# Kernel optimization log

Measured on AMD Instinct MI355X. Metric: run time of the kernel, lower is better.

The kernel has to match this reference:

```python
import jax, jax.numpy as jnp
import numpy as np

D = 4096  # input_size
H = 4096  # hidden_size


def setup_inputs() -> dict:
    key = jax.random.key(0)
    ks = jax.random.split(key, 18)
    inp = {
        "x": jax.random.normal(ks[0], (D,), jnp.float32),
        "h_prev": jax.random.normal(ks[1], (H,), jnp.float32),
        "c_prev": jax.random.normal(ks[2], (H, H), jnp.float32),
        "n_prev": jax.random.normal(ks[3], (H,), jnp.float32),
        "m_prev": jax.random.normal(ks[4], (H,), jnp.float32),
    }
    names = ["q", "k", "v", "i", "f", "o"]
    for idx, nm in enumerate(names):
        inp[f"W{nm}"] = jax.random.normal(ks[5 + 2 * idx], (H, D), jnp.float32) * 0.02
        inp[f"b{nm}"] = jax.random.normal(ks[6 + 2 * idx], (H,), jnp.float32) * 0.02
    return inp


def reference(x, h_prev, c_prev, n_prev, m_prev,
              Wq, bq, Wk, bk, Wv, bv, Wi, bi, Wf, bf, Wo, bo):
    # Six linear projections (nn.Linear: W @ x + b for 1-D x)
    q = Wq @ x + bq
    k = (Wk @ x + bk) / jnp.sqrt(jnp.float32(H))
    v = Wv @ x + bv
    o = jax.nn.sigmoid(Wo @ x + bo)
    i_tilde = Wi @ x + bi
    f_tilde = Wf @ x + bf

    # Stabilizer state and exp gates
    m_t = jnp.maximum(f_tilde + m_prev, i_tilde)          # [H]
    i_g = jnp.exp(i_tilde - m_t)                          # [H]
    f_g = jnp.exp(f_tilde + m_prev - m_t)                 # [H]

    # Rank-1 outer-product state update; gates broadcast over last axis (as in torch)
    c_t = f_g * c_prev + i_g * jnp.outer(v, k)            # [H, H]
    n_t = f_g * n_prev + i_g * k                          # [H]

    # Normalized matvec output
    denom = jnp.maximum(jnp.abs(jnp.dot(n_t, q)), jnp.float32(1.0))
    h_t = o * (c_t @ q) / denom                           # [H]
    return (h_t, c_t, n_t, m_t)
```

## Files before the change

### kernel.cpp

```cpp
#include <hip/hip_runtime.h>
#include <math.h>

#define HD 4096

__global__ __launch_bounds__(256, 6) void k_gemv(
    const float* __restrict__ x,
    const float* __restrict__ Wq, const float* __restrict__ Wk,
    const float* __restrict__ Wv, const float* __restrict__ Wi,
    const float* __restrict__ Wf, const float* __restrict__ Wo,
    float* __restrict__ ws_dots)
{
    __shared__ float xs[HD];
    const int tid = threadIdx.x;
    {
        const float4* x4  = (const float4*)x;
        float4*       sx4 = (float4*)xs;
#pragma unroll
        for (int i = 0; i < 4; ++i) sx4[i * 256 + tid] = x4[i * 256 + tid];
    }
    __syncthreads();

    const int wave = tid >> 6;
    const int lane = tid & 63;
    const int mat  = blockIdx.x >> 10;
    const int row  = ((blockIdx.x & 1023) << 2) | wave;

    const float* W = Wq;
    if      (mat == 1) W = Wk;
    else if (mat == 2) W = Wv;
    else if (mat == 3) W = Wi;
    else if (mat == 4) W = Wf;
    else if (mat == 5) W = Wo;

    const float4* Wrow = (const float4*)(W + (size_t)row * HD) + lane;
    const float4* sx4  = (const float4*)xs + lane;

    float a0 = 0.f, a1 = 0.f;
#pragma unroll
    for (int t = 0; t < 16; t += 2) {
        float4 w0 = Wrow[t * 64];
        float4 x0 = sx4[t * 64];
        float4 w1 = Wrow[(t + 1) * 64];
        float4 x1 = sx4[(t + 1) * 64];
        a0 += w0.x * x0.x + w0.y * x0.y + w0.z * x0.z + w0.w * x0.w;
        a1 += w1.x * x1.x + w1.y * x1.y + w1.z * x1.z + w1.w * x1.w;
    }
    float acc = a0 + a1;
#pragma unroll
    for (int off = 32; off > 0; off >>= 1)
        acc += __shfl_xor(acc, off, 64);

    if (lane == 0) ws_dots[(mat << 12) | row] = acc;
}

__global__ __launch_bounds__(256) void k_gates(
    const float* __restrict__ ws_dots,
    const float* __restrict__ bq, const float* __restrict__ bk,
    const float* __restrict__ bv, const float* __restrict__ bi,
    const float* __restrict__ bf, const float* __restrict__ bo,
    const float* __restrict__ n_prev, const float* __restrict__ m_prev,
    float* __restrict__ ws_q, float* __restrict__ ws_v,
    float* __restrict__ ws_o, float* __restrict__ ws_fg,
    float* __restrict__ ws_ik,
    float* __restrict__ out_n, float* __restrict__ out_m,
    float* __restrict__ ws_nq)
{
    const int tid = threadIdx.x;
    const int row = blockIdx.x * 256 + tid;

    float dq  = ws_dots[0 * HD + row];
    float dk  = ws_dots[1 * HD + row];
    float dv  = ws_dots[2 * HD + row];
    float di  = ws_dots[3 * HD + row];
    float df  = ws_dots[4 * HD + row];
    float d_o = ws_dots[5 * HD + row];

    float q  = dq + bq[row];
    float k  = (dk + bk[row]) * (1.0f / 64.0f);
    float v  = dv + bv[row];
    float o  = 1.0f / (1.0f + expf(-(d_o + bo[row])));
    float it = di + bi[row];
    float ft = df + bf[row];
    float mp = m_prev[row];
    float mt = fmaxf(ft + mp, it);
    float ig = expf(it - mt);
    float fg = expf(ft + mp - mt);
    float nt = fg * n_prev[row] + ig * k;

    ws_q[row]  = q;
    ws_v[row]  = v;
    ws_o[row]  = o;
    ws_fg[row] = fg;
    ws_ik[row] = ig * k;
    out_n[row] = nt;
    out_m[row] = mt;

    float acc = nt * q;
#pragma unroll
    for (int off = 32; off > 0; off >>= 1)
        acc += __shfl_xor(acc, off, 64);
    __shared__ float red[4];
    if ((tid & 63) == 0) red[tid >> 6] = acc;
    __syncthreads();
    if (tid == 0) ws_nq[blockIdx.x] = red[0] + red[1] + red[2] + red[3];
}

__global__ __launch_bounds__(256) void k_ct(
    const float* __restrict__ c_prev,
    const float* __restrict__ ws_q, const float* __restrict__ ws_v,
    const float* __restrict__ ws_o, const float* __restrict__ ws_fg,
    const float* __restrict__ ws_ik, const float* __restrict__ ws_nq,
    float* __restrict__ out_h, float* __restrict__ out_c)
{
    const int row = blockIdx.x;
    const int tid = threadIdx.x;
    const float vr = ws_v[row];

    const float4* cp4 = (const float4*)(c_prev + (size_t)row * HD);
    float4*       ct4 = (float4*)(out_c + (size_t)row * HD);
    const float4* fg4 = (const float4*)ws_fg;
    const float4* ik4 = (const float4*)ws_ik;
    const float4* q4  = (const float4*)ws_q;

    float4 c[4], f[4], k[4], qv[4];
#pragma unroll
    for (int t = 0; t < 4; ++t) {
        const int idx = t * 256 + tid;
        c[t]  = cp4[idx];
        f[t]  = fg4[idx];
        k[t]  = ik4[idx];
        qv[t] = q4[idx];
    }

    float acc = 0.f;
#pragma unroll
    for (int t = 0; t < 4; ++t) {
        const int idx = t * 256 + tid;
        float4 ct;
        ct.x = f[t].x * c[t].x + k[t].x * vr;
        ct.y = f[t].y * c[t].y + k[t].y * vr;
        ct.z = f[t].z * c[t].z + k[t].z * vr;
        ct.w = f[t].w * c[t].w + k[t].w * vr;
        ct4[idx] = ct;
        acc += ct.x * qv[t].x + ct.y * qv[t].y + ct.z * qv[t].z + ct.w * qv[t].w;
    }
#pragma unroll
    for (int off = 32; off > 0; off >>= 1)
        acc += __shfl_xor(acc, off, 64);
    __shared__ float red[4];
    if ((tid & 63) == 0) red[tid >> 6] = acc;
    __syncthreads();
    if (tid == 0) {
        float s = red[0] + red[1] + red[2] + red[3];
        float d = 0.f;
#pragma unroll
        for (int i = 0; i < 16; ++i) d += ws_nq[i];
        float den = fmaxf(fabsf(d), 1.0f);
        out_h[row] = ws_o[row] * s / den;
    }
}

extern "C" void kernel_launch(void* const* d_in, const int* in_sizes, int n_in,
                              void* d_out, int out_size, void* d_ws, size_t ws_size,
                              hipStream_t stream) {
    const float* x      = (const float*)d_in[0];
    const float* c_prev = (const float*)d_in[2];
    const float* n_prev = (const float*)d_in[3];
    const float* m_prev = (const float*)d_in[4];
    const float* Wq = (const float*)d_in[5];  const float* bq = (const float*)d_in[6];
    const float* Wk = (const float*)d_in[7];  const float* bk = (const float*)d_in[8];
    const float* Wv = (const float*)d_in[9];  const float* bv = (const float*)d_in[10];
    const float* Wi = (const float*)d_in[11]; const float* bi = (const float*)d_in[12];
    const float* Wf = (const float*)d_in[13]; const float* bf = (const float*)d_in[14];
    const float* Wo = (const float*)d_in[15]; const float* bo = (const float*)d_in[16];

    float* out   = (float*)d_out;
    float* out_h = out;
    float* out_c = out + HD;
    float* out_n = out + HD + (size_t)HD * HD;
    float* out_m = out_n + HD;

    float* ws      = (float*)d_ws;
    float* ws_dots = ws;
    float* ws_q    = ws + 6 * HD;
    float* ws_v    = ws + 7 * HD;
    float* ws_o    = ws + 8 * HD;
    float* ws_fg   = ws + 9 * HD;
    float* ws_ik   = ws + 10 * HD;
    float* ws_nq   = ws + 11 * HD;

    k_gemv<<<6 * 1024, 256, 0, stream>>>(x, Wq, Wk, Wv, Wi, Wf, Wo, ws_dots);
    k_gates<<<16, 256, 0, stream>>>(ws_dots, bq, bk, bv, bi, bf, bo,
                                    n_prev, m_prev,
                                    ws_q, ws_v, ws_o, ws_fg, ws_ik,
                                    out_n, out_m, ws_nq);
    k_ct<<<HD, 256, 0, stream>>>(c_prev, ws_q, ws_v, ws_o, ws_fg, ws_ik,
                                 ws_nq, out_h, out_c);
}
```

Before: 437.1 us.

## Stream GEMV weights through double-buffered LDS via direct global-to-LDS loads

The projection GEMV now gives each wave four rows and keeps x in registers instead of shared memory. Weight chunks are streamed into per-wave double-buffered LDS with global_load_lds, using explicit waitcnt so the next chunk loads while the current one is reduced. The grid shrinks from 6144 to 1536 blocks and the launch-bounds occupancy hint drops from 6 to 4. This raises register use (16 float4 of x per thread) and relies on hand-written waitcnt ordering, which is fragile.

```diff
diff --git a/kernel.cpp b/kernel.cpp
--- a/kernel.cpp
+++ b/kernel.cpp
@@ -3,27 +3,27 @@
 
 #define HD 4096
 
-__global__ __launch_bounds__(256, 6) void k_gemv(
+__device__ __forceinline__ void gload16(const float* g, float* l) {
+    __builtin_amdgcn_global_load_lds(
+        (const __attribute__((address_space(1))) void*)g,
+        (__attribute__((address_space(3))) void*)l,
+        16, 0, 0);
+}
+
+__global__ __launch_bounds__(256, 4) void k_gemv(
     const float* __restrict__ x,
     const float* __restrict__ Wq, const float* __restrict__ Wk,
     const float* __restrict__ Wv, const float* __restrict__ Wi,
     const float* __restrict__ Wf, const float* __restrict__ Wo,
     float* __restrict__ ws_dots)
 {
-    __shared__ float xs[HD];
-    const int tid = threadIdx.x;
-    {
-        const float4* x4  = (const float4*)x;
-        float4*       sx4 = (float4*)xs;
-#pragma unroll
-        for (int i = 0; i < 4; ++i) sx4[i * 256 + tid] = x4[i * 256 + tid];
-    }
-    __syncthreads();
-
+    __shared__ float buf[4][2][1024];
+    const int tid  = threadIdx.x;
     const int wave = tid >> 6;
     const int lane = tid & 63;
-    const int mat  = blockIdx.x >> 10;
-    const int row  = ((blockIdx.x & 1023) << 2) | wave;
+    const int mat  = blockIdx.x >> 8;
+    const int base = (blockIdx.x & 255) << 4;
+    const int srow = base + (wave << 2);
 
     const float* W = Wq;
     if      (mat == 1) W = Wk;
@@ -32,25 +32,53 @@
     else if (mat == 4) W = Wf;
     else if (mat == 5) W = Wo;
 
-    const float4* Wrow = (const float4*)(W + (size_t)row * HD) + lane;
-    const float4* sx4  = (const float4*)xs + lane;
-
-    float a0 = 0.f, a1 = 0.f;
-#pragma unroll
-    for (int t = 0; t < 16; t += 2) {
-        float4 w0 = Wrow[t * 64];
-        float4 x0 = sx4[t * 64];
-        float4 w1 = Wrow[(t + 1) * 64];
-        float4 x1 = sx4[(t + 1) * 64];
-        a0 += w0.x * x0.x + w0.y * x0.y + w0.z * x0.z + w0.w * x0.w;
-        a1 += w1.x * x1.x + w1.y * x1.y + w1.z * x1.z + w1.w * x1.w;
-    }
-    float acc = a0 + a1;
-#pragma unroll
-    for (int off = 32; off > 0; off >>= 1)
-        acc += __shfl_xor(acc, off, 64);
-
-    if (lane == 0) ws_dots[(mat << 12) | row] = acc;
+    const float* Ws = W + (size_t)srow * HD;
+
+    const float4* x4 = (const float4*)x;
+    float4 xr[16];
+#pragma unroll
+    for (int k = 0; k < 16; ++k)
+        xr[k] = x4[((k >> 2) << 8) + ((k & 3) << 6) + lane];
+
+    float* mybuf = &buf[wave][0][0];
+
+#pragma unroll
+    for (int j = 0; j < 4; ++j)
+        gload16(Ws + (j << 8) + (lane << 2), mybuf + (j << 8));
+
+    float acc = 0.f;
+#pragma unroll
+    for (int c = 0; c < 16; ++c) {
+        asm volatile("s_waitcnt lgkmcnt(0)" ::: "memory");
+        if (c < 15) {
+            const float* src = Ws + ((c + 1) << 10) + (lane << 2);
+            float*       dst = mybuf + (((c + 1) & 1) << 10);
+#pragma unroll
+            for (int j = 0; j < 4; ++j)
+                gload16(src + (j << 8), dst + (j << 8));
+            asm volatile("s_waitcnt vmcnt(4)" ::: "memory");
+        } else {
+            asm volatile("s_waitcnt vmcnt(0)" ::: "memory");
+        }
+
+        const float* cb = mybuf + ((c & 1) << 10);
+#pragma unroll
+        for (int j = 0; j < 4; ++j) {
+            float4 w  = *(const float4*)(cb + (j << 8) + (lane << 2));
+            float4 xv = xr[((c & 3) << 2) + j];
+            acc += w.x * xv.x + w.y * xv.y + w.z * xv.z + w.w * xv.w;
+        }
+
+        if ((c & 3) == 3) {
+            float r = acc;
+#pragma unroll
+            for (int off = 32; off > 0; off >>= 1)
+                r += __shfl_xor(r, off, 64);
+            if (lane == 0)
+                ws_dots[(mat << 12) | (srow + (c >> 2))] = r;
+            acc = 0.f;
+        }
+    }
 }
 
 __global__ __launch_bounds__(256) void k_gates(
@@ -145,8 +173,7 @@
         acc += ct.x * qv[t].x + ct.y * qv[t].y + ct.z * qv[t].z + ct.w * qv[t].w;
     }
 #pragma unroll
-    for (int off = 32; off > 0; off >>= 1)
-        acc += __shfl_xor(acc, off, 64);
+    for (int off = 32; off > 0; off >>= 1) acc += __shfl_xor(acc, off, 64);
     __shared__ float red[4];
     if ((tid & 63) == 0) red[tid >> 6] = acc;
     __syncthreads();
@@ -189,7 +216,7 @@
     float* ws_ik   = ws + 10 * HD;
     float* ws_nq   = ws + 11 * HD;
 
-    k_gemv<<<6 * 1024, 256, 0, stream>>>(x, Wq, Wk, Wv, Wi, Wf, Wo, ws_dots);
+    k_gemv<<<1536, 256, 0, stream>>>(x, Wq, Wk, Wv, Wi, Wf, Wo, ws_dots);
     k_gates<<<16, 256, 0, stream>>>(ws_dots, bq, bk, bv, bi, bf, bo,
                                     n_prev, m_prev,
                                     ws_q, ws_v, ws_o, ws_fg, ws_ik,
```

After: 443.4 us. About the same (+1.5%).
